# Kernel optimization log

Measured on AMD Instinct MI355X. Metric: run time of the kernel, lower is better.

The kernel has to match this reference:

```python
import jax, jax.numpy as jnp
import numpy as np

D_MODEL = 1024
N_HEAD = 16
D_K = D_MODEL // N_HEAD
FFN = 4096
EPS = 1e-5


def layer_norm(x, g, b):
    mu = jnp.mean(x, axis=-1, keepdims=True)
    var = jnp.var(x, axis=-1, keepdims=True)
    return (x - mu) * jax.lax.rsqrt(var + EPS) * g + b


def setup_inputs() -> dict:
    key = jax.random.key(0)
    ks = jax.random.split(key, 16)
    B, L = 2, 2048
    s = 1.0 / np.sqrt(D_MODEL)
    inp = {
        "x": jax.random.normal(ks[0], (B, L, D_MODEL), dtype=jnp.float32),
        "mask": jnp.ones((B, 1, 1, L), dtype=jnp.int32),
        "ln1_g": jnp.ones((D_MODEL,), jnp.float32),
        "ln1_b": jnp.zeros((D_MODEL,), jnp.float32),
        "Wq": jax.random.normal(ks[1], (D_MODEL, D_MODEL), jnp.float32) * s,
        "bq": jnp.zeros((D_MODEL,), jnp.float32),
        "Wk": jax.random.normal(ks[2], (D_MODEL, D_MODEL), jnp.float32) * s,
        "bk": jnp.zeros((D_MODEL,), jnp.float32),
        "Wv": jax.random.normal(ks[3], (D_MODEL, D_MODEL), jnp.float32) * s,
        "bv": jnp.zeros((D_MODEL,), jnp.float32),
        "Wo": jax.random.normal(ks[4], (D_MODEL, D_MODEL), jnp.float32) * s,
        "bo": jnp.zeros((D_MODEL,), jnp.float32),
        "ln2_g": jnp.ones((D_MODEL,), jnp.float32),
        "ln2_b": jnp.zeros((D_MODEL,), jnp.float32),
        "W1": jax.random.normal(ks[5], (D_MODEL, FFN), jnp.float32) * s,
        "b1": jnp.zeros((FFN,), jnp.float32),
        "W2": jax.random.normal(ks[6], (FFN, D_MODEL), jnp.float32) * (1.0 / np.sqrt(FFN)),
        "b2": jnp.zeros((D_MODEL,), jnp.float32),
    }
    return inp


def reference(x, mask, ln1_g, ln1_b, Wq, bq, Wk, bk, Wv, bv, Wo, bo,
              ln2_g, ln2_b, W1, b1, W2, b2):
    B, L, _ = x.shape
    nx = layer_norm(x, ln1_g, ln1_b)
    # QKV projections, split heads -> [B, H, L, Dk]
    def proj(W, b):
        return (nx @ W + b).reshape(B, L, N_HEAD, D_K).transpose(0, 2, 1, 3)
    q, k, v = proj(Wq, bq), proj(Wk, bk), proj(Wv, bv)
    scores = jnp.einsum('bhqd,bhkd->bhqk', q, k) / np.sqrt(D_K)
    scores = jnp.where(mask.astype(bool), scores, -jnp.inf)
    attn = jax.nn.softmax(scores, axis=-1)
    out = jnp.einsum('bhqk,bhkd->bhqd', attn, v)
    out = out.transpose(0, 2, 1, 3).reshape(B, L, D_MODEL)
    out = out @ Wo + bo
    x = x + out  # residual (dropout p=0)
    nx = layer_norm(x, ln2_g, ln2_b)
    h = jax.nn.silu(nx @ W1 + b1)
    x = x + (h @ W2 + b2)
    return x
```

## Files before the change

kernel.cpp:

```cpp
#include <hip/hip_runtime.h>
#include <hip/hip_bf16.h>

#define D_MODEL 1024
#define N_HEAD  16
#define D_K     64
#define FFN_DIM 4096
#define B_SZ    2
#define L_SEQ   2048
#define ROWS    (B_SZ * L_SEQ)
#define PST     68

typedef float  floatx4 __attribute__((ext_vector_type(4)));
typedef short  shortx8 __attribute__((ext_vector_type(8)));

__device__ __forceinline__ unsigned short f2bf(float f) {
    unsigned int u = __float_as_uint(f);
    unsigned int rounding = 0x7fffu + ((u >> 16) & 1u);
    return (unsigned short)((u + rounding) >> 16);
}
__device__ __forceinline__ float bf2f(unsigned short u) {
    return __uint_as_float(((unsigned int)u) << 16);
}

__device__ __forceinline__ void glds16(const unsigned short* g, unsigned short* l) {
    __builtin_amdgcn_global_load_lds(
        (const __attribute__((address_space(1))) unsigned int*)g,
        (__attribute__((address_space(3))) unsigned int*)l, 16, 0, 0);
}

__device__ __forceinline__ void xcd_remap_gemm(int& bx, int& by, int& bz) {
    const int gx = gridDim.x, gy = gridDim.y, gz = gridDim.z;
    const int o = blockIdx.x + gx * (blockIdx.y + gy * blockIdx.z);
    const int nwg = gx * gy * gz;
    const int t = (o & 7) * (nwg >> 3) + (o >> 3);
    const int zsz = gx * gy;
    bz = t / zsz;
    const int w = t - bz * zsz;
    const int grp = w / (8 * gy);
    const int in  = w - grp * (8 * gy);
    by = in >> 3;
    bx = grp * 8 + (in & 7);
}

__global__ __launch_bounds__(256) void ln_kernel(const float* __restrict__ x,
                                                 const float* __restrict__ g,
                                                 const float* __restrict__ b,
                                                 unsigned short* __restrict__ out) {
    const int row = blockIdx.x;
    const int tid = threadIdx.x;
    const float* xr = x + (size_t)row * D_MODEL;
    float4 xv = *reinterpret_cast<const float4*>(&xr[tid * 4]);
    float v[4] = {xv.x, xv.y, xv.z, xv.w};
    float s = v[0] + v[1] + v[2] + v[3];
    float ss = v[0] * v[0] + v[1] * v[1] + v[2] * v[2] + v[3] * v[3];
    __shared__ float r1[256], r2[256];
    r1[tid] = s; r2[tid] = ss;
    __syncthreads();
    for (int off = 128; off > 0; off >>= 1) {
        if (tid < off) { r1[tid] += r1[tid + off]; r2[tid] += r2[tid + off]; }
        __syncthreads();
    }
    const float mean = r1[0] * (1.0f / D_MODEL);
    const float var  = r2[0] * (1.0f / D_MODEL) - mean * mean;
    const float inv  = rsqrtf(var + 1e-5f);
    unsigned short* orow = out + (size_t)row * D_MODEL;
    ushort4 o;
    o.x = f2bf((v[0] - mean) * inv * g[tid * 4 + 0] + b[tid * 4 + 0]);
    o.y = f2bf((v[1] - mean) * inv * g[tid * 4 + 1] + b[tid * 4 + 1]);
    o.z = f2bf((v[2] - mean) * inv * g[tid * 4 + 2] + b[tid * 4 + 2]);
    o.w = f2bf((v[3] - mean) * inv * g[tid * 4 + 3] + b[tid * 4 + 3]);
    *reinterpret_cast<ushort4*>(&orow[tid * 4]) = o;
}

__global__ __launch_bounds__(256) void transpose_cast(const float* __restrict__ W,
                                                      unsigned short* __restrict__ Wt,
                                                      int K, int N) {
    __shared__ unsigned short T[32][33];
    const int t = threadIdx.x;
    const int k0 = blockIdx.y * 32, n0 = blockIdx.x * 32;
    const int kr = t >> 3, nc = (t & 7) * 4;
    float4 w = *reinterpret_cast<const float4*>(&W[(size_t)(k0 + kr) * N + n0 + nc]);
    T[kr][nc + 0] = f2bf(w.x); T[kr][nc + 1] = f2bf(w.y);
    T[kr][nc + 2] = f2bf(w.z); T[kr][nc + 3] = f2bf(w.w);
    __syncthreads();
    const int nr = t >> 3, kc = (t & 7) * 4;
    ushort4 o;
    o.x = T[kc + 0][nr]; o.y = T[kc + 1][nr];
    o.z = T[kc + 2][nr]; o.w = T[kc + 3][nr];
    *reinterpret_cast<ushort4*>(&Wt[(size_t)(n0 + nr) * K + k0 + kc]) = o;
}

__global__ __launch_bounds__(256) void transpose_cast4(const float* s0, const float* s1,
                                                       const float* s2, const float* s3,
                                                       unsigned short* d0, unsigned short* d1,
                                                       unsigned short* d2, unsigned short* d3) {
    const int z = blockIdx.z;
    const float* W = (z == 0) ? s0 : (z == 1) ? s1 : (z == 2) ? s2 : s3;
    unsigned short* Wt = (z == 0) ? d0 : (z == 1) ? d1 : (z == 2) ? d2 : d3;
    __shared__ unsigned short T[32][33];
    const int t = threadIdx.x;
    const int k0 = blockIdx.y * 32, n0 = blockIdx.x * 32;
    const int kr = t >> 3, nc = (t & 7) * 4;
    float4 w = *reinterpret_cast<const float4*>(&W[(size_t)(k0 + kr) * D_MODEL + n0 + nc]);
    T[kr][nc + 0] = f2bf(w.x); T[kr][nc + 1] = f2bf(w.y);
    T[kr][nc + 2] = f2bf(w.z); T[kr][nc + 3] = f2bf(w.w);
    __syncthreads();
    const int nr = t >> 3, kc = (t & 7) * 4;
    ushort4 o;
    o.x = T[kc + 0][nr]; o.y = T[kc + 1][nr];
    o.z = T[kc + 2][nr]; o.w = T[kc + 3][nr];
    *reinterpret_cast<ushort4*>(&Wt[(size_t)(n0 + nr) * D_MODEL + k0 + kc]) = o;
}


#define GEMM_STAGE(AS, BS, KT)                                            \
    do {                                                                  \
        glds16(A  + sA0 + (KT), &AS[p0 * 8]);                             \
        glds16(A  + sA1 + (KT), &AS[p1 * 8]);                             \
        glds16(Wt + sB0 + (KT), &BS[p0 * 8]);                             \
        glds16(Wt + sB1 + (KT), &BS[p1 * 8]);                             \
    } while (0)

#define GEMM_COMPUTE(AS, BS)                                              \
    do {                                                                  \
        shortx8 af[4], bf[4];                                             \
        _Pragma("unroll")                                                 \
        for (int i = 0; i < 4; ++i)                                       \
            af[i] = *reinterpret_cast<const shortx8*>(&AS[offA[i]]);      \
        _Pragma("unroll")                                                 \
        for (int j = 0; j < 4; ++j)                                       \
            bf[j] = *reinterpret_cast<const shortx8*>(&BS[offB[j]]);      \
        _Pragma("unroll")                                                 \
        for (int i = 0; i < 4; ++i)                                       \
            _Pragma("unroll")                                             \
            for (int j = 0; j < 4; ++j)                                   \
                acc[i][j] = __builtin_amdgcn_mfma_f32_16x16x32_bf16(af[i], bf[j], acc[i][j], 0, 0, 0); \
    } while (0)

#define GEMM_PREAMBLE                                                     \
    const int tid  = threadIdx.x;                                         \
    const int lane = tid & 63;                                            \
    const int wave = tid >> 6;                                            \
    int bx, by, bz;                                                       \
    xcd_remap_gemm(bx, by, bz);                                           \
    const int row0 = by * 128, col0 = bx * 128;                           \
    const int wr = (wave >> 1) * 64, wc = (wave & 1) * 64;                \
    floatx4 acc[4][4] = {};                                               \
    const int p0 = tid,       r0s = p0 >> 2, k0s = (((p0 & 3) - (r0s >> 1)) & 3) * 8; \
    const int p1 = tid + 256, r1s = p1 >> 2, k1s = (((p1 & 3) - (r1s >> 1)) & 3) * 8; \
    const int am = (lane & 15);                                           \
    const size_t sA0 = (size_t)(row0 + r0s) * K + k0s;                    \
    const size_t sA1 = (size_t)(row0 + r1s) * K + k1s;                    \
    const size_t sB0 = (size_t)(col0 + r0s) * K + k0s;                    \
    const size_t sB1 = (size_t)(col0 + r1s) * K + k1s;                    \
    int offA[4], offB[4];                                                 \
    _Pragma("unroll")                                                     \
    for (int i = 0; i < 4; ++i) {                                         \
        const int Ra = wr + i * 16 + am;                                  \
        offA[i] = Ra * 32 + (((lane >> 4) + (Ra >> 1)) & 3) * 8;          \
        const int Rb = wc + i * 16 + am;                                  \
        offB[i] = Rb * 32 + (((lane >> 4) + (Rb >> 1)) & 3) * 8;          \
    }

template <int SILU, int HAS_RES, int OUT_BF16>
__global__ __launch_bounds__(256) void mfma_gemm(const unsigned short* __restrict__ A,
                                                 const unsigned short* __restrict__ Wt,
                                                 const float* __restrict__ bias,
                                                 const float* __restrict__ res,
                                                 void* __restrict__ outP,
                                                 int M, int N, int K) {
    __shared__ unsigned short As0[128 * 32], As1[128 * 32];
    __shared__ unsigned short Bs0[128 * 32], Bs1[128 * 32];
    GEMM_PREAMBLE

    GEMM_STAGE(As0, Bs0, 0);
    __syncthreads();
    for (int kt = 0; kt < K; kt += 64) {
        GEMM_STAGE(As1, Bs1, kt + 32);
        GEMM_COMPUTE(As0, Bs0);
        __syncthreads();
        if (kt + 64 < K) GEMM_STAGE(As0, Bs0, kt + 64);
        GEMM_COMPUTE(As1, Bs1);
        __syncthreads();
    }

    const int cq = (lane >> 4) * 4;
    const int cn = lane & 15;
#pragma unroll
    for (int i = 0; i < 4; ++i) {
#pragma unroll
        for (int j = 0; j < 4; ++j) {
            const int n = col0 + wc + j * 16 + cn;
            const float bb = bias[n];
#pragma unroll
            for (int r = 0; r < 4; ++r) {
                const int m = row0 + wr + i * 16 + cq + r;
                float v = acc[i][j][r] + bb;
                if (SILU) v = v / (1.0f + __expf(-v));
                if (HAS_RES) v += res[(size_t)m * N + n];
                if (OUT_BF16) ((unsigned short*)outP)[(size_t)m * N + n] = f2bf(v);
                else          ((float*)outP)[(size_t)m * N + n] = v;
            }
        }
    }
}

__global__ __launch_bounds__(256) void mfma_gemm_qkv(const unsigned short* __restrict__ A,
                                                     const unsigned short* __restrict__ Wt,
                                                     const float* __restrict__ bq,
                                                     const float* __restrict__ bk,
                                                     const float* __restrict__ bv,
                                                     unsigned short* __restrict__ qb,
                                                     unsigned short* __restrict__ kb,
                                                     unsigned short* __restrict__ vtb) {
    const int K = D_MODEL, M = ROWS;
    __shared__ unsigned short As0[128 * 32], As1[128 * 32];
    __shared__ unsigned short Bs0[128 * 32], Bs1[128 * 32];
    GEMM_PREAMBLE

    GEMM_STAGE(As0, Bs0, 0);
    __syncthreads();
    for (int kt = 0; kt < K; kt += 64) {
        GEMM_STAGE(As1, Bs1, kt + 32);
        GEMM_COMPUTE(As0, Bs0);
        __syncthreads();
        if (kt + 64 < K) GEMM_STAGE(As0, Bs0, kt + 64);
        GEMM_COMPUTE(As1, Bs1);
        __syncthreads();
    }

    const int cq = (lane >> 4) * 4;
    const int cn = lane & 15;
    const int sel = col0 >> 10;
    const int nbase = col0 & 1023;
    const float* bias = (sel == 0) ? bq : (sel == 1) ? bk : bv;
    const float scl = (sel == 0) ? 0.18033688511157292f : 1.0f;
#pragma unroll
    for (int i = 0; i < 4; ++i) {
#pragma unroll
        for (int j = 0; j < 4; ++j) {
            const int n = nbase + wc + j * 16 + cn;
            const float bb = bias[n];
            if (sel == 2) {
                const int m0 = row0 + wr + i * 16 + cq;
                ushort4 o;
                o.x = f2bf(acc[i][j][0] + bb);
                o.y = f2bf(acc[i][j][1] + bb);
                o.z = f2bf(acc[i][j][2] + bb);
                o.w = f2bf(acc[i][j][3] + bb);
                *reinterpret_cast<ushort4*>(&vtb[(size_t)n * M + m0]) = o;
            } else {
                unsigned short* dst = (sel == 0) ? qb : kb;
#pragma unroll
                for (int r = 0; r < 4; ++r) {
                    const int m = row0 + wr + i * 16 + cq + r;
                    dst[(size_t)m * D_MODEL + n] = f2bf((acc[i][j][r] + bb) * scl);
                }
            }
        }
    }
}

__global__ __launch_bounds__(256) void mfma_gemm_splitk(const unsigned short* __restrict__ A,
                                                        const unsigned short* __restrict__ Wt,
                                                        unsigned short* __restrict__ parts,
                                                        int M, int N, int KS) {
    __shared__ unsigned short As0[128 * 32], As1[128 * 32];
    __shared__ unsigned short Bs0[128 * 32], Bs1[128 * 32];
    const int K = KS * gridDim.z;
    GEMM_PREAMBLE
    const int kbeg = bz * KS;
    unsigned short* outp = parts + (size_t)bz * M * N;

    GEMM_STAGE(As0, Bs0, kbeg);
    __syncthreads();
    for (int kt = kbeg; kt < kbeg + KS; kt += 64) {
        GEMM_STAGE(As1, Bs1, kt + 32);
        GEMM_COMPUTE(As0, Bs0);
        __syncthreads();
        if (kt + 64 < kbeg + KS) GEMM_STAGE(As0, Bs0, kt + 64);
        GEMM_COMPUTE(As1, Bs1);
        __syncthreads();
    }

    const int cq = (lane >> 4) * 4;
    const int cn = lane & 15;
#pragma unroll
    for (int i = 0; i < 4; ++i)
#pragma unroll
        for (int j = 0; j < 4; ++j) {
            const int n = col0 + wc + j * 16 + cn;
#pragma unroll
            for (int r = 0; r < 4; ++r) {
                const int m = row0 + wr + i * 16 + cq + r;
                outp[(size_t)m * N + n] = f2bf(acc[i][j][r]);
            }
        }
}

__global__ __launch_bounds__(256) void combine_kernel(const unsigned short* __restrict__ p0,
                                                      const unsigned short* __restrict__ p1,
                                                      const float* __restrict__ bias,
                                                      const float* __restrict__ res,
                                                      float* __restrict__ out) {
    const size_t e0 = ((size_t)blockIdx.x * 256 + threadIdx.x) * 4;
    const int col = (int)(e0 & 1023);
    ushort4 a = *reinterpret_cast<const ushort4*>(&p0[e0]);
    ushort4 b = *reinterpret_cast<const ushort4*>(&p1[e0]);
    float4 r = *reinterpret_cast<const float4*>(&res[e0]);
    float4 o;
    o.x = bf2f(a.x) + bf2f(b.x) + bias[col + 0] + r.x;
    o.y = bf2f(a.y) + bf2f(b.y) + bias[col + 1] + r.y;
    o.z = bf2f(a.z) + bf2f(b.z) + bias[col + 2] + r.z;
    o.w = bf2f(a.w) + bf2f(b.w) + bias[col + 3] + r.w;
    *reinterpret_cast<float4*>(&out[e0]) = o;
}

__global__ __launch_bounds__(512) void attn_mfma(const unsigned short* __restrict__ Q,
                                                 const unsigned short* __restrict__ K,
                                                 const unsigned short* __restrict__ Vt,
                                                 const int* __restrict__ mask,
                                                 unsigned short* __restrict__ att) {
    const int tid  = threadIdx.x;
    const int lane = tid & 63;
    const int wave = tid >> 6;
    const int o = blockIdx.x + gridDim.x * (blockIdx.y + gridDim.y * blockIdx.z);
    const int nwg = gridDim.x * gridDim.y * gridDim.z;
    const int t = (o & 7) * (nwg >> 3) + (o >> 3);
    const int qx = t % gridDim.x;
    const int h  = (t / gridDim.x) % gridDim.y;
    const int b  = t / (gridDim.x * gridDim.y);
    const int q0 = qx * 128;

    __shared__ unsigned short Qs[128 * PST];
    __shared__ unsigned short Ks[2][64 * 64];
    __shared__ unsigned short Vs[2][64 * 64];
    __shared__ unsigned short Ps[128 * PST];
    __shared__ unsigned char mkb[128];

    const int am = lane & 15;
    const int aq = (lane >> 4) * 8;
    const int cq = (lane >> 4) * 4;
    const int cn = lane & 15;

    for (int c = tid; c < 1024; c += 512) {
        const int r = c >> 3, off = (c & 7) * 8;
        *reinterpret_cast<uint4*>(&Qs[r * PST + off]) =
            *reinterpret_cast<const uint4*>(&Q[(size_t)(b * L_SEQ + q0 + r) * D_MODEL + h * D_K + off]);
    }

    const int p0 = tid, sr0 = p0 >> 3, sc0 = (((p0 & 7) - sr0) & 7) * 8;
    const unsigned short* K0 = K + (size_t)(b * L_SEQ + sr0) * D_MODEL + h * D_K + sc0;
    const unsigned short* V0 = Vt + (size_t)(h * D_K + sr0) * ROWS + b * L_SEQ + sc0;

    int offF[2][4];
#pragma unroll
    for (int kt = 0; kt < 2; ++kt)
#pragma unroll
        for (int tt = 0; tt < 4; ++tt) {
            const int R = tt * 16 + am;
            offF[kt][tt] = R * 64 + (((kt * 4 + (lane >> 4)) + R) & 7) * 8;
        }

    __syncthreads();

    shortx8 aQ[2];
    aQ[0] = *reinterpret_cast<const shortx8*>(&Qs[(wave * 16 + am) * PST + aq]);
    aQ[1] = *reinterpret_cast<const shortx8*>(&Qs[(wave * 16 + am) * PST + 32 + aq]);

    floatx4 oacc[4] = {};
    float lsum = 0.0f;

    for (int j0 = 0; j0 < L_SEQ; j0 += 128) {
        __syncthreads();
        glds16(K0 + (size_t)j0 * D_MODEL,        &Ks[0][p0 * 8]);
        glds16(K0 + (size_t)(j0 + 64) * D_MODEL, &Ks[1][p0 * 8]);
        glds16(V0 + j0,      &Vs[0][p0 * 8]);
        glds16(V0 + j0 + 64, &Vs[1][p0 * 8]);
        if (tid < 128) mkb[tid] = (unsigned char)(mask[b * L_SEQ + j0 + tid] != 0);
        __syncthreads();

#pragma unroll
        for (int u = 0; u < 2; ++u) {
            floatx4 sacc[4] = {};
#pragma unroll
            for (int kt = 0; kt < 2; ++kt)
#pragma unroll
                for (int jt = 0; jt < 4; ++jt) {
                    shortx8 bK = *reinterpret_cast<const shortx8*>(&Ks[u][offF[kt][jt]]);
                    sacc[jt] = __builtin_amdgcn_mfma_f32_16x16x32_bf16(bK, aQ[kt], sacc[jt], 0, 0, 0);
                }
#pragma unroll
            for (int jt = 0; jt < 4; ++jt) {
                uchar4 mb = *reinterpret_cast<const uchar4*>(&mkb[u * 64 + jt * 16 + cq]);
                float pv0 = mb.x ? __builtin_amdgcn_exp2f(sacc[jt][0]) : 0.0f;
                float pv1 = mb.y ? __builtin_amdgcn_exp2f(sacc[jt][1]) : 0.0f;
                float pv2 = mb.z ? __builtin_amdgcn_exp2f(sacc[jt][2]) : 0.0f;
                float pv3 = mb.w ? __builtin_amdgcn_exp2f(sacc[jt][3]) : 0.0f;
                lsum += (pv0 + pv1) + (pv2 + pv3);
                unsigned int pk0, pk1;
                asm("v_cvt_pk_bf16_f32 %0, %1, %2" : "=v"(pk0) : "v"(pv0), "v"(pv1));
                asm("v_cvt_pk_bf16_f32 %0, %1, %2" : "=v"(pk1) : "v"(pv2), "v"(pv3));
                uint2 w; w.x = pk0; w.y = pk1;
                *reinterpret_cast<uint2*>(&Ps[(wave * 16 + cn) * PST + jt * 16 + cq]) = w;
            }
#pragma unroll
            for (int kt = 0; kt < 2; ++kt) {
                shortx8 aP = *reinterpret_cast<const shortx8*>(&Ps[(wave * 16 + am) * PST + kt * 32 + aq]);
#pragma unroll
                for (int dt = 0; dt < 4; ++dt) {
                    shortx8 bV = *reinterpret_cast<const shortx8*>(&Vs[u][offF[kt][dt]]);
                    oacc[dt] = __builtin_amdgcn_mfma_f32_16x16x32_bf16(aP, bV, oacc[dt], 0, 0, 0);
                }
            }
        }
    }

    float lt = lsum;
    lt += __shfl_xor(lt, 16);
    lt += __shfl_xor(lt, 32);
    float linv[4];
#pragma unroll
    for (int r = 0; r < 4; ++r)
        linv[r] = 1.0f / __shfl(lt, cq + r);

#pragma unroll
    for (int dt = 0; dt < 4; ++dt)
#pragma unroll
        for (int r = 0; r < 4; ++r) {
            att[(size_t)(b * L_SEQ + q0 + wave * 16 + cq + r) * D_MODEL + h * D_K + dt * 16 + cn] =
                f2bf(oacc[dt][r] * linv[r]);
        }
}

extern "C" void kernel_launch(void* const* d_in, const int* in_sizes, int n_in,
                              void* d_out, int out_size, void* d_ws, size_t ws_size,
                              hipStream_t stream) {
    const float* x     = (const float*)d_in[0];
    const int*   mask  = (const int*)d_in[1];
    const float* ln1_g = (const float*)d_in[2];
    const float* ln1_b = (const float*)d_in[3];
    const float* Wq    = (const float*)d_in[4];
    const float* bq    = (const float*)d_in[5];
    const float* Wk    = (const float*)d_in[6];
    const float* bk    = (const float*)d_in[7];
    const float* Wv    = (const float*)d_in[8];
    const float* bv    = (const float*)d_in[9];
    const float* Wo    = (const float*)d_in[10];
    const float* bo    = (const float*)d_in[11];
    const float* ln2_g = (const float*)d_in[12];
    const float* ln2_b = (const float*)d_in[13];
    const float* W1    = (const float*)d_in[14];
    const float* b1    = (const float*)d_in[15];
    const float* W2    = (const float*)d_in[16];
    const float* b2    = (const float*)d_in[17];
    float* out = (float*)d_out;

    float* ws = (float*)d_ws;
    const size_t SZ = (size_t)ROWS * D_MODEL;

    unsigned short* nx  = (unsigned short*)(ws + 0 * SZ);
    unsigned short* qb  = (unsigned short*)(ws + 1 * SZ);
    unsigned short* kb  = qb + SZ;
    unsigned short* vtb = (unsigned short*)(ws + 2 * SZ);
    unsigned short* attb = vtb + SZ;
    float* x1  = out;
    unsigned short* nx2 = nx;
    unsigned short* h = (unsigned short*)(ws + 2 * SZ);
    unsigned short* parts = (unsigned short*)(ws + 0 * SZ);

    unsigned short* WqkvT = (unsigned short*)(ws + 4 * SZ);
    unsigned short* WqT = WqkvT;
    unsigned short* WkT = WqkvT + (size_t)D_MODEL * D_MODEL;
    unsigned short* WvT = WkT + (size_t)D_MODEL * D_MODEL;
    unsigned short* WoT = WvT + (size_t)D_MODEL * D_MODEL;
    unsigned short* W1T = (unsigned short*)(ws + 1 * SZ);
    unsigned short* W2T = W1T + (size_t)D_MODEL * FFN_DIM;

    ln_kernel<<<ROWS, 256, 0, stream>>>(x, ln1_g, ln1_b, nx);

    transpose_cast4<<<dim3(32, 32, 4), 256, 0, stream>>>(Wq, Wk, Wv, Wo, WqT, WkT, WvT, WoT);

    mfma_gemm_qkv<<<dim3(3072 / 128, ROWS / 128), 256, 0, stream>>>(
        nx, WqkvT, bq, bk, bv, qb, kb, vtb);

    attn_mfma<<<dim3(L_SEQ / 128, N_HEAD, B_SZ), 512, 0, stream>>>(qb, kb, vtb, mask, attb);

    transpose_cast<<<dim3(FFN_DIM / 32, D_MODEL / 32), 256, 0, stream>>>(W1, W1T, D_MODEL, FFN_DIM);
    transpose_cast<<<dim3(D_MODEL / 32, FFN_DIM / 32), 256, 0, stream>>>(W2, W2T, FFN_DIM, D_MODEL);

    mfma_gemm<0, 1, 0><<<dim3(D_MODEL / 128, ROWS / 128), 256, 0, stream>>>(
        attb, WoT, bo, x, x1, ROWS, D_MODEL, D_MODEL);

    ln_kernel<<<ROWS, 256, 0, stream>>>(x1, ln2_g, ln2_b, nx2);

    mfma_gemm<1, 0, 1><<<dim3(FFN_DIM / 128, ROWS / 128), 256, 0, stream>>>(
        nx2, W1T, b1, nullptr, h, ROWS, FFN_DIM, D_MODEL);

    mfma_gemm_splitk<<<dim3(D_MODEL / 128, ROWS / 128, 2), 256, 0, stream>>>(
        h, W2T, parts, ROWS, D_MODEL, FFN_DIM / 2);
    combine_kernel<<<(ROWS * D_MODEL) / 1024, 256, 0, stream>>>(
        parts, parts + SZ, b2, x1, out);
}
```

Baseline: 364.1 us.

## Split key tiles across wave groups in attention and halve query tile

```diff
diff --git a/kernel.cpp b/kernel.cpp
--- a/kernel.cpp
+++ b/kernel.cpp
@@ -324,28 +324,33 @@
     const int tid  = threadIdx.x;
     const int lane = tid & 63;
     const int wave = tid >> 6;
+    const int u    = wave >> 2;
+    const int s    = wave & 3;
     const int o = blockIdx.x + gridDim.x * (blockIdx.y + gridDim.y * blockIdx.z);
     const int nwg = gridDim.x * gridDim.y * gridDim.z;
     const int t = (o & 7) * (nwg >> 3) + (o >> 3);
     const int qx = t % gridDim.x;
     const int h  = (t / gridDim.x) % gridDim.y;
     const int b  = t / (gridDim.x * gridDim.y);
-    const int q0 = qx * 128;
-
-    __shared__ unsigned short Qs[128 * PST];
-    __shared__ unsigned short Ks[2][64 * 64];
-    __shared__ unsigned short Vs[2][64 * 64];
-    __shared__ unsigned short Ps[128 * PST];
+    const int q0 = qx * 64;
+
+    __shared__ unsigned short QPs0[64 * PST];
+    __shared__ unsigned short Ps1[64 * PST];
+    __shared__ __align__(16) unsigned char BIG[32768];
     __shared__ unsigned char mkb[128];
+    __shared__ float lr[8][16];
+
+    unsigned short* S = (unsigned short*)BIG;
+    float* red = (float*)BIG;
 
     const int am = lane & 15;
     const int aq = (lane >> 4) * 8;
     const int cq = (lane >> 4) * 4;
     const int cn = lane & 15;
 
-    for (int c = tid; c < 1024; c += 512) {
-        const int r = c >> 3, off = (c & 7) * 8;
-        *reinterpret_cast<uint4*>(&Qs[r * PST + off]) =
+    {
+        const int r = tid >> 3, off = (tid & 7) * 8;
+        *reinterpret_cast<uint4*>(&QPs0[r * PST + off]) =
             *reinterpret_cast<const uint4*>(&Q[(size_t)(b * L_SEQ + q0 + r) * D_MODEL + h * D_K + off]);
     }
 
@@ -362,56 +367,57 @@
             offF[kt][tt] = R * 64 + (((kt * 4 + (lane >> 4)) + R) & 7) * 8;
         }
 
+    unsigned short* KsU = S + u * 4096;
+    unsigned short* VsU = S + 8192 + u * 4096;
+    unsigned short* PsU = (u == 0) ? QPs0 : Ps1;
+
     __syncthreads();
 
     shortx8 aQ[2];
-    aQ[0] = *reinterpret_cast<const shortx8*>(&Qs[(wave * 16 + am) * PST + aq]);
-    aQ[1] = *reinterpret_cast<const shortx8*>(&Qs[(wave * 16 + am) * PST + 32 + aq]);
+    aQ[0] = *reinterpret_cast<const shortx8*>(&QPs0[(s * 16 + am) * PST + aq]);
+    aQ[1] = *reinterpret_cast<const shortx8*>(&QPs0[(s * 16 + am) * PST + 32 + aq]);
 
     floatx4 oacc[4] = {};
     float lsum = 0.0f;
 
     for (int j0 = 0; j0 < L_SEQ; j0 += 128) {
         __syncthreads();
-        glds16(K0 + (size_t)j0 * D_MODEL,        &Ks[0][p0 * 8]);
-        glds16(K0 + (size_t)(j0 + 64) * D_MODEL, &Ks[1][p0 * 8]);
-        glds16(V0 + j0,      &Vs[0][p0 * 8]);
-        glds16(V0 + j0 + 64, &Vs[1][p0 * 8]);
+        glds16(K0 + (size_t)j0 * D_MODEL,        &S[p0 * 8]);
+        glds16(K0 + (size_t)(j0 + 64) * D_MODEL, &S[4096 + p0 * 8]);
+        glds16(V0 + j0,      &S[8192 + p0 * 8]);
+        glds16(V0 + j0 + 64, &S[12288 + p0 * 8]);
         if (tid < 128) mkb[tid] = (unsigned char)(mask[b * L_SEQ + j0 + tid] != 0);
         __syncthreads();
 
-#pragma unroll
-        for (int u = 0; u < 2; ++u) {
-            floatx4 sacc[4] = {};
-#pragma unroll
-            for (int kt = 0; kt < 2; ++kt)
-#pragma unroll
-                for (int jt = 0; jt < 4; ++jt) {
-                    shortx8 bK = *reinterpret_cast<const shortx8*>(&Ks[u][offF[kt][jt]]);
-                    sacc[jt] = __builtin_amdgcn_mfma_f32_16x16x32_bf16(bK, aQ[kt], sacc[jt], 0, 0, 0);
-                }
+        floatx4 sacc[4] = {};
+#pragma unroll
+        for (int kt = 0; kt < 2; ++kt)
 #pragma unroll
             for (int jt = 0; jt < 4; ++jt) {
-                uchar4 mb = *reinterpret_cast<const uchar4*>(&mkb[u * 64 + jt * 16 + cq]);
-                float pv0 = mb.x ? __builtin_amdgcn_exp2f(sacc[jt][0]) : 0.0f;
-                float pv1 = mb.y ? __builtin_amdgcn_exp2f(sacc[jt][1]) : 0.0f;
-                float pv2 = mb.z ? __builtin_amdgcn_exp2f(sacc[jt][2]) : 0.0f;
-                float pv3 = mb.w ? __builtin_amdgcn_exp2f(sacc[jt][3]) : 0.0f;
-                lsum += (pv0 + pv1) + (pv2 + pv3);
-                unsigned int pk0, pk1;
-                asm("v_cvt_pk_bf16_f32 %0, %1, %2" : "=v"(pk0) : "v"(pv0), "v"(pv1));
-                asm("v_cvt_pk_bf16_f32 %0, %1, %2" : "=v"(pk1) : "v"(pv2), "v"(pv3));
-                uint2 w; w.x = pk0; w.y = pk1;
-                *reinterpret_cast<uint2*>(&Ps[(wave * 16 + cn) * PST + jt * 16 + cq]) = w;
+                shortx8 bK = *reinterpret_cast<const shortx8*>(&KsU[offF[kt][jt]]);
+                sacc[jt] = __builtin_amdgcn_mfma_f32_16x16x32_bf16(bK, aQ[kt], sacc[jt], 0, 0, 0);
             }
 #pragma unroll
-            for (int kt = 0; kt < 2; ++kt) {
-                shortx8 aP = *reinterpret_cast<const shortx8*>(&Ps[(wave * 16 + am) * PST + kt * 32 + aq]);
-#pragma unroll
-                for (int dt = 0; dt < 4; ++dt) {
-                    shortx8 bV = *reinterpret_cast<const shortx8*>(&Vs[u][offF[kt][dt]]);
-                    oacc[dt] = __builtin_amdgcn_mfma_f32_16x16x32_bf16(aP, bV, oacc[dt], 0, 0, 0);
-                }
+        for (int jt = 0; jt < 4; ++jt) {
+            uchar4 mb = *reinterpret_cast<const uchar4*>(&mkb[u * 64 + jt * 16 + cq]);
+            float pv0 = mb.x ? __builtin_amdgcn_exp2f(sacc[jt][0]) : 0.0f;
+            float pv1 = mb.y ? __builtin_amdgcn_exp2f(sacc[jt][1]) : 0.0f;
+            float pv2 = mb.z ? __builtin_amdgcn_exp2f(sacc[jt][2]) : 0.0f;
+            float pv3 = mb.w ? __builtin_amdgcn_exp2f(sacc[jt][3]) : 0.0f;
+            lsum += (pv0 + pv1) + (pv2 + pv3);
+            unsigned int pk0, pk1;
+            asm("v_cvt_pk_bf16_f32 %0, %1, %2" : "=v"(pk0) : "v"(pv0), "v"(pv1));
+            asm("v_cvt_pk_bf16_f32 %0, %1, %2" : "=v"(pk1) : "v"(pv2), "v"(pv3));
+            uint2 w; w.x = pk0; w.y = pk1;
+            *reinterpret_cast<uint2*>(&PsU[(s * 16 + cn) * PST + jt * 16 + cq]) = w;
+        }
+#pragma unroll
+        for (int kt = 0; kt < 2; ++kt) {
+            shortx8 aP = *reinterpret_cast<const shortx8*>(&PsU[(s * 16 + am) * PST + kt * 32 + aq]);
+#pragma unroll
+            for (int dt = 0; dt < 4; ++dt) {
+                shortx8 bV = *reinterpret_cast<const shortx8*>(&VsU[offF[kt][dt]]);
+                oacc[dt] = __builtin_amdgcn_mfma_f32_16x16x32_bf16(aP, bV, oacc[dt], 0, 0, 0);
             }
         }
     }
@@ -419,18 +425,34 @@
     float lt = lsum;
     lt += __shfl_xor(lt, 16);
     lt += __shfl_xor(lt, 32);
-    float linv[4];
-#pragma unroll
-    for (int r = 0; r < 4; ++r)
-        linv[r] = 1.0f / __shfl(lt, cq + r);
-
-#pragma unroll
-    for (int dt = 0; dt < 4; ++dt)
-#pragma unroll
-        for (int r = 0; r < 4; ++r) {
-            att[(size_t)(b * L_SEQ + q0 + wave * 16 + cq + r) * D_MODEL + h * D_K + dt * 16 + cn] =
-                f2bf(oacc[dt][r] * linv[r]);
-        }
+
+    __syncthreads();
+    if (u == 1) {
+#pragma unroll
+        for (int dt = 0; dt < 4; ++dt)
+#pragma unroll
+            for (int r = 0; r < 4; ++r)
+                red[(s * 16 + cq + r) * 66 + dt * 16 + cn] = oacc[dt][r];
+        if (lane < 16) lr[wave][lane] = lt;
+    } else {
+        if (lane < 16) lr[wave][lane] = lt;
+    }
+    __syncthreads();
+
+    if (u == 0) {
+        float linv[4];
+#pragma unroll
+        for (int r = 0; r < 4; ++r)
+            linv[r] = 1.0f / (lr[s][cq + r] + lr[s + 4][cq + r]);
+#pragma unroll
+        for (int dt = 0; dt < 4; ++dt)
+#pragma unroll
+            for (int r = 0; r < 4; ++r) {
+                float tot = oacc[dt][r] + red[(s * 16 + cq + r) * 66 + dt * 16 + cn];
+                att[(size_t)(b * L_SEQ + q0 + s * 16 + cq + r) * D_MODEL + h * D_K + dt * 16 + cn] =
+                    f2bf(tot * linv[r]);
+            }
+    }
 }
 
 extern "C" void kernel_launch(void* const* d_in, const int* in_sizes, int n_in,
@@ -484,7 +506,7 @@
     mfma_gemm_qkv<<<dim3(3072 / 128, ROWS / 128), 256, 0, stream>>>(
         nx, WqkvT, bq, bk, bv, qb, kb, vtb);
 
-    attn_mfma<<<dim3(L_SEQ / 128, N_HEAD, B_SZ), 512, 0, stream>>>(qb, kb, vtb, mask, attb);
+    attn_mfma<<<dim3(L_SEQ / 64, N_HEAD, B_SZ), 512, 0, stream>>>(qb, kb, vtb, mask, attb);
 
     transpose_cast<<<dim3(FFN_DIM / 32, D_MODEL / 32), 256, 0, stream>>>(W1, W1T, D_MODEL, FFN_DIM);
     transpose_cast<<<dim3(D_MODEL / 32, FFN_DIM / 32), 256, 0, stream>>>(W2, W2T, FFN_DIM, D_MODEL);
```

Result: slower. 389.3 us (+6.9%).
